# Kernel optimization log

Hardware: AMD Instinct MI355X
Metric: run time of the kernel (lower is better)

The kernel has to match this reference:

```python
import jax, jax.numpy as jnp
import numpy as np

DIM = 320; D_STATE = 32; D_CONV = 4; HEADDIM = 80; D_INNER = 640; NHEADS = 8
CONV_DIM = D_INNER + 2 * D_STATE          # 704
D_IN_PROJ = 2 * D_INNER + 2 * D_STATE + NHEADS  # 1352
ATTN_HEADS = 4; MLP_DIM = 1024; DEPTH = 2; INNER = DIM // 2  # cross-attn downsample_rate=2
PATCH = (128.0, 256.0, 256.0); IMG = (16, 32, 32); NPTS = 6; BATCH = 2
EPS = 1e-5
TWO_PI = 2.0 * np.pi


def layernorm(x, w, b):
    m = x.mean(-1, keepdims=True)
    v = ((x - m) ** 2).mean(-1, keepdims=True)
    return (x - m) * jax.lax.rsqrt(v + EPS) * w + b


def pe_encode(coords, gauss):
    # coords in [0,1], last dim 3 -> random fourier features (sin|cos) of width DIM
    c = TWO_PI * ((2.0 * coords - 1.0) @ gauss)
    return jnp.concatenate([jnp.sin(c), jnp.cos(c)], -1)


def mha(qi, ki, vi, wq, bq, wk, bk, wv, bv, wo, bo):
    q = qi @ wq.T + bq
    k = ki @ wk.T + bk
    v = vi @ wv.T + bv
    B, Nq, Ci = q.shape
    hd = Ci // ATTN_HEADS
    q = q.reshape(B, Nq, ATTN_HEADS, hd)
    k = k.reshape(B, -1, ATTN_HEADS, hd)
    v = v.reshape(B, -1, ATTN_HEADS, hd)
    att = jax.nn.softmax(jnp.einsum('bqhd,bkhd->bhqk', q, k) / np.sqrt(hd), -1)
    o = jnp.einsum('bhqk,bkhd->bqhd', att, v).reshape(B, Nq, Ci)
    return o @ wo.T + bo


def mamba2(xn, in_w, conv_w, conv_b, dt_bias, A_log, Dp, rms_w, out_w):
    Bt, L, _ = xn.shape
    zxbcdt = xn @ in_w.T                                    # (B,L,1352)
    z, xBC, dt = jnp.split(zxbcdt, [D_INNER, D_INNER + CONV_DIM], axis=-1)
    dt = jax.nn.softplus(dt + dt_bias)                      # (B,L,H)
    # causal depthwise conv over sequence, kernel D_CONV
    pad = jnp.pad(xBC, ((0, 0), (D_CONV - 1, 0), (0, 0)))
    conv = conv_b + sum(pad[:, k:k + L] * conv_w[:, k] for k in range(D_CONV))
    xBC = jax.nn.silu(conv)
    xs, Bm, Cm = jnp.split(xBC, [D_INNER, D_INNER + D_STATE], axis=-1)
    A = -jnp.exp(A_log)                                     # (H,)
    xh = xs.reshape(Bt, L, NHEADS, HEADDIM)

    def step(S, inp):  # S: (B,H,N,P)
        dt_t, x_t, B_t, C_t = inp  # (B,H),(B,H,P),(B,N),(B,N)
        decay = jnp.exp(dt_t * A)
        S = S * decay[..., None, None] + (dt_t[..., None, None] * B_t[:, None, :, None]) * x_t[:, :, None, :]
        y = jnp.einsum('bn,bhnp->bhp', C_t, S)
        return S, y

    S0 = jnp.zeros((Bt, NHEADS, D_STATE, HEADDIM), xn.dtype)
    _, ys = jax.lax.scan(step, S0, (dt.transpose(1, 0, 2), xh.transpose(1, 0, 2, 3), Bm.transpose(1, 0, 2), Cm.transpose(1, 0, 2)))
    y = ys.transpose(1, 0, 2, 3) + Dp[None, None, :, None] * xh  # (B,L,H,P)
    y = y.reshape(Bt, L, D_INNER)
    y = y * jax.nn.silu(z)                                  # gated RMSNorm (norm_before_gate=False)
    y = y * jax.lax.rsqrt((y * y).mean(-1, keepdims=True) + EPS) * rms_w
    return y @ out_w.T


def _forward(x, coords, ln_w, ln_b, in_w, conv_w, conv_b, dt_bias, A_log, Dp, rms_w, out_w,
             pe_gauss, point_tab, sa_w, sa_b, t2i_w, t2i_b, t2i_ow, t2i_ob,
             i2t_w, i2t_b, i2t_ow, i2t_ob, norms_w, norms_b, mlp_w1, mlp_b1, mlp_w2, mlp_b2, labels):
    B, C = x.shape[:2]
    img = x.shape[2:]
    n = int(np.prod(img))
    xf = jnp.transpose(x.reshape(B, C, n), (0, 2, 1))       # (B,n,C)
    keys = mamba2(layernorm(xf, ln_w, ln_b), in_w, conv_w, conv_b, dt_bias, A_log, Dp, rms_w, out_w)
    # point embeddings: fourier PE of normalized click coords + label embedding
    point_emb = pe_encode(coords / jnp.asarray(PATCH, x.dtype), pe_gauss) + point_tab[labels]
    # dense image positional encoding over the feature grid
    axes = [(jnp.arange(s, dtype=x.dtype) + 0.5) / s for s in img]
    grid = jnp.stack(jnp.meshgrid(*axes, indexing='ij'), -1)  # (d,h,w,3)
    kpe = jnp.broadcast_to(pe_encode(grid, pe_gauss).reshape(1, n, C), (B, n, C))
    queries = point_emb
    qpe = point_emb
    for i in range(DEPTH):
        saw, sab = sa_w[i], sa_b[i]
        if i == 0:  # skip_first_layer_pe
            queries = mha(queries, queries, queries, saw[0], sab[0], saw[1], sab[1], saw[2], sab[2], saw[3], sab[3])
        else:
            q = queries + qpe
            queries = queries + mha(q, q, queries, saw[0], sab[0], saw[1], sab[1], saw[2], sab[2], saw[3], sab[3])
        queries = layernorm(queries, norms_w[i, 0], norms_b[i, 0])
        q = queries + qpe
        k = keys + kpe
        queries = queries + mha(q, k, keys, t2i_w[i, 0], t2i_b[i, 0], t2i_w[i, 1], t2i_b[i, 1], t2i_w[i, 2], t2i_b[i, 2], t2i_ow[i], t2i_ob[i])
        queries = layernorm(queries, norms_w[i, 1], norms_b[i, 1])
        queries = queries + jax.nn.relu(queries @ mlp_w1[i].T + mlp_b1[i]) @ mlp_w2[i].T + mlp_b2[i]
        queries = layernorm(queries, norms_w[i, 2], norms_b[i, 2])
        q = queries + qpe
        k = keys + kpe
        keys = keys + mha(k, q, queries, i2t_w[i, 0], i2t_b[i, 0], i2t_w[i, 1], i2t_b[i, 1], i2t_w[i, 2], i2t_b[i, 2], i2t_ow[i], i2t_ob[i])
        keys = layernorm(keys, norms_w[i, 3], norms_b[i, 3])
    return jnp.transpose(keys, (0, 2, 1)).reshape(B, C, *img)


def setup_inputs():
    key = jax.random.key(0)
    ks = iter(jax.random.split(key, 64))
    f32 = jnp.float32

    def nrm(shape, s=0.02):
        return s * jax.random.normal(next(ks), shape, dtype=f32)

    inp = {}
    inp['x'] = jax.random.normal(next(ks), (BATCH, DIM) + IMG, dtype=f32)
    inp['coords'] = jax.random.uniform(next(ks), (BATCH, NPTS, 3), dtype=f32) * jnp.asarray(PATCH, f32)
    inp['labels'] = jax.random.randint(next(ks), (BATCH, NPTS), 0, 2)
    inp['ln_w'] = jnp.ones((DIM,), f32)
    inp['ln_b'] = jnp.zeros((DIM,), f32)
    inp['in_w'] = nrm((D_IN_PROJ, DIM))
    inp['conv_w'] = nrm((CONV_DIM, D_CONV), 0.2)
    inp['conv_b'] = jnp.zeros((CONV_DIM,), f32)
    inp['dt_bias'] = nrm((NHEADS,), 0.1)
    inp['A_log'] = jnp.log(jnp.arange(1, NHEADS + 1, dtype=f32))
    inp['Dp'] = jnp.ones((NHEADS,), f32)
    inp['rms_w'] = jnp.ones((D_INNER,), f32)
    inp['out_w'] = nrm((DIM, D_INNER))
    inp['pe_gauss'] = jax.random.normal(next(ks), (3, DIM // 2), dtype=f32)
    inp['point_tab'] = nrm((2, DIM), 1.0)
    inp['sa_w'] = nrm((DEPTH, 4, DIM, DIM))
    inp['sa_b'] = jnp.zeros((DEPTH, 4, DIM), f32)
    inp['t2i_w'] = nrm((DEPTH, 3, INNER, DIM))
    inp['t2i_b'] = jnp.zeros((DEPTH, 3, INNER), f32)
    inp['t2i_ow'] = nrm((DEPTH, DIM, INNER))
    inp['t2i_ob'] = jnp.zeros((DEPTH, DIM), f32)
    inp['i2t_w'] = nrm((DEPTH, 3, INNER, DIM))
    inp['i2t_b'] = jnp.zeros((DEPTH, 3, INNER), f32)
    inp['i2t_ow'] = nrm((DEPTH, DIM, INNER))
    inp['i2t_ob'] = jnp.zeros((DEPTH, DIM), f32)
    inp['norms_w'] = jnp.ones((DEPTH, 4, DIM), f32)
    inp['norms_b'] = jnp.zeros((DEPTH, 4, DIM), f32)
    inp['mlp_w1'] = nrm((DEPTH, MLP_DIM, DIM))
    inp['mlp_b1'] = jnp.zeros((DEPTH, MLP_DIM), f32)
    inp['mlp_w2'] = nrm((DEPTH, DIM, MLP_DIM))
    inp['mlp_b2'] = jnp.zeros((DEPTH, DIM), f32)
    return inp


def reference(x, coords, labels, ln_w, ln_b, in_w, conv_w, conv_b, dt_bias, A_log, Dp, rms_w, out_w,
              pe_gauss, point_tab, sa_w, sa_b, t2i_w, t2i_b, t2i_ow, t2i_ob,
              i2t_w, i2t_b, i2t_ow, i2t_ob, norms_w, norms_b, mlp_w1, mlp_b1, mlp_w2, mlp_b2):
    return _forward(x, coords, ln_w, ln_b, in_w, conv_w, conv_b, dt_bias, A_log, Dp, rms_w, out_w,
                    pe_gauss, point_tab, sa_w, sa_b, t2i_w, t2i_b, t2i_ow, t2i_ob,
                    i2t_w, i2t_b, i2t_ow, i2t_ob, norms_w, norms_b, mlp_w1, mlp_b1, mlp_w2, mlp_b2, labels)
```

## Files before the change

### kernel.cpp

```cpp
#include <hip/hip_runtime.h>
#include <math.h>

#define LSEQ 16384
#define CDIM 320
#define DIN 640
#define NHH 8
#define CONVD 704
#define XBCW 712
#define QCH 64
#define NCHUNK 256

typedef __bf16 bf16_t;
typedef __bf16 bf16x8 __attribute__((ext_vector_type(8)));
typedef __bf16 bf16x4 __attribute__((ext_vector_type(4)));
typedef float f32x4 __attribute__((ext_vector_type(4)));

__device__ __forceinline__ float wave_sum(float v) {
#pragma unroll
  for (int o = 32; o > 0; o >>= 1) v += __shfl_down(v, o, 64);
  return v;
}
__device__ __forceinline__ float wave_max(float v) {
#pragma unroll
  for (int o = 32; o > 0; o >>= 1) v = fmaxf(v, __shfl_down(v, o, 64));
  return v;
}
__device__ __forceinline__ float block_sum256(float v, float* red) {
  int tid = threadIdx.x;
  v = wave_sum(v);
  __syncthreads();
  if ((tid & 63) == 0) red[tid >> 6] = v;
  __syncthreads();
  return red[0] + red[1] + red[2] + red[3];
}

__global__ void ws_probe(float* out, float v) { out[0] = v; }

__global__ void cvt_bf(const float* __restrict__ src, bf16_t* __restrict__ dst, int n) {
  int i = (blockIdx.x * 256 + threadIdx.x) * 4;
  if (i >= n) return;
  float4 v = *(const float4*)(src + i);
  bf16x4 o;
  o[0] = (bf16_t)v.x; o[1] = (bf16_t)v.y; o[2] = (bf16_t)v.z; o[3] = (bf16_t)v.w;
  *(bf16x4*)(dst + i) = o;
}

__global__ __launch_bounds__(256) void tln(const float* __restrict__ x,
                                           const float* __restrict__ w,
                                           const float* __restrict__ b,
                                           bf16_t* __restrict__ out) {
  __shared__ float sT[32][321];
  int t0 = blockIdx.x * 32;
  int tid = threadIdx.x;
  for (int i = tid; i < 2560; i += 256) {
    int c = i >> 3, j4 = i & 7;
    float4 v = *(const float4*)(x + (size_t)c * LSEQ + t0 + j4 * 4);
    sT[j4 * 4 + 0][c] = v.x;
    sT[j4 * 4 + 1][c] = v.y;
    sT[j4 * 4 + 2][c] = v.z;
    sT[j4 * 4 + 3][c] = v.w;
  }
  __syncthreads();
  int wave = tid >> 6, lane = tid & 63;
  for (int tt = wave; tt < 32; tt += 4) {
    float xv[5];
    float s = 0.f;
#pragma unroll
    for (int k = 0; k < 5; ++k) { xv[k] = sT[tt][lane + 64 * k]; s += xv[k]; }
    s = wave_sum(s); s = __shfl(s, 0, 64);
    float mean = s * (1.f / 320.f);
    float v = 0.f;
#pragma unroll
    for (int k = 0; k < 5; ++k) { float d = xv[k] - mean; v += d * d; }
    v = wave_sum(v); v = __shfl(v, 0, 64);
    float rstd = rsqrtf(v * (1.f / 320.f) + 1e-5f);
    bf16_t* op = out + (size_t)(t0 + tt) * CDIM;
#pragma unroll
    for (int k = 0; k < 5; ++k) {
      int i = lane + 64 * k;
      op[i] = (bf16_t)((xv[k] - mean) * rstd * w[i] + b[i]);
    }
  }
}

__global__ __launch_bounds__(256) void lnt(const float* __restrict__ in,
                                           const float* __restrict__ w,
                                           const float* __restrict__ b,
                                           float* __restrict__ out) {
  __shared__ float sT[CDIM][33];
  int t0 = blockIdx.x * 32;
  int tid = threadIdx.x;
  int wave = tid >> 6, lane = tid & 63;
  for (int tt = wave; tt < 32; tt += 4) {
    const float* xp = in + (size_t)(t0 + tt) * CDIM;
    float x[5];
    float s = 0.f;
#pragma unroll
    for (int k = 0; k < 5; ++k) { x[k] = xp[lane + 64 * k]; s += x[k]; }
    s = wave_sum(s); s = __shfl(s, 0, 64);
    float mean = s * (1.f / 320.f);
    float v = 0.f;
#pragma unroll
    for (int k = 0; k < 5; ++k) { float d = x[k] - mean; v += d * d; }
    v = wave_sum(v); v = __shfl(v, 0, 64);
    float rstd = rsqrtf(v * (1.f / 320.f) + 1e-5f);
#pragma unroll
    for (int k = 0; k < 5; ++k) {
      int i = lane + 64 * k;
      sT[i][tt] = (x[k] - mean) * rstd * w[i] + b[i];
    }
  }
  __syncthreads();
  for (int i = tid; i < 320 * 32; i += 256) {
    int cc = i >> 5, t = i & 31;
    out[(size_t)cc * LSEQ + t0 + t] = sT[cc][t];
  }
}

__global__ __launch_bounds__(256) void ln_rows256(float* __restrict__ io,
                                                  const float* __restrict__ w,
                                                  const float* __restrict__ b,
                                                  int nrows) {
  int row = blockIdx.x * 4 + (threadIdx.x >> 6);
  if (row >= nrows) return;
  float* xp = io + (size_t)row * CDIM;
  int lane = threadIdx.x & 63;
  float x[5];
  float s = 0.f;
#pragma unroll
  for (int k = 0; k < 5; ++k) { x[k] = xp[lane + 64 * k]; s += x[k]; }
  s = wave_sum(s); s = __shfl(s, 0, 64);
  float mean = s * (1.f / 320.f);
  float v = 0.f;
#pragma unroll
  for (int k = 0; k < 5; ++k) { float t = x[k] - mean; v += t * t; }
  v = wave_sum(v); v = __shfl(v, 0, 64);
  float rstd = rsqrtf(v * (1.f / 320.f) + 1e-5f);
#pragma unroll
  for (int k = 0; k < 5; ++k) {
    int i = lane + 64 * k;
    xp[i] = (x[k] - mean) * rstd * w[i] + b[i];
  }
}

__global__ __launch_bounds__(256) void gemm64(
    const void* __restrict__ A, const void* __restrict__ W,
    const float* __restrict__ bias, const float* __restrict__ pe,
    void* __restrict__ C, void* __restrict__ C2,
    const void* __restrict__ W2, const float* __restrict__ bias2, int wsplit,
    int M, int N, int K, int lda, int ldc, int nsplit, int ldc2,
    int addC, int abf, int wbf, int cbf, long long sA, long long sC) {
  int z = blockIdx.z;
  int gx = gridDim.x;
  int nwg = gx * gridDim.y;
  int lin = blockIdx.y * gx + blockIdx.x;
  int xcd = lin & 7, idx = lin >> 3;
  int q = nwg >> 3, r = nwg & 7;
  int base = (xcd < r) ? xcd * (q + 1) : r * (q + 1) + (xcd - r) * q;
  int lin2 = base + idx;
  int mblk = lin2 / gx, nblk = lin2 % gx;
  int m0 = mblk << 6, n0 = nblk << 6;

  __shared__ __align__(16) bf16_t As[2][2048];
  __shared__ __align__(16) bf16_t Ws[2][2048];
  int tid = threadIdx.x;
  int wave = tid >> 6, lane = tid & 63;
  int fm = lane & 15, quad = lane >> 4;
  int rA = tid >> 2, qA = tid & 3;
  const float* ag = nullptr;
  const bf16_t* agb = nullptr;
  const float* peg = nullptr;
  if (abf) {
    agb = (const bf16_t*)A + (size_t)z * sA + (size_t)(m0 + rA) * lda + qA * 8;
  } else {
    ag = (const float*)A + (size_t)z * sA + (size_t)(m0 + rA) * lda + qA * 8;
    if (pe) peg = pe + (size_t)(m0 + rA) * lda + qA * 8;
  }
  int wRow = n0 + rA;
  bool wok = wRow < N;
  const float* wg = nullptr;
  const bf16_t* wgb = nullptr;
  {
    const void* Wsel = (wRow < wsplit) ? W : W2;
    int wr = (wRow < wsplit) ? wRow : wRow - wsplit;
    if (wbf) wgb = (const bf16_t*)Wsel + (size_t)wr * K + qA * 8;
    else     wg  = (const float*)Wsel + (size_t)wr * K + qA * 8;
  }
  int off = (rA >> 4) * 512 + (qA * 16 + (rA & 15)) * 8;

  f32x4 acc[4];
#pragma unroll
  for (int j = 0; j < 4; ++j) acc[j] = (f32x4){0.f, 0.f, 0.f, 0.f};

  bf16x8 ra, rw;
  float4 pa0, pa1, pw0, pw1;
  auto loadG = [&](int k0) {
    if (abf) {
      ra = *(const bf16x8*)(agb + k0);
    } else {
      pa0 = *(const float4*)(ag + k0);
      pa1 = *(const float4*)(ag + k0 + 4);
      if (peg) {
        float4 q0 = *(const float4*)(peg + k0);
        float4 q1 = *(const float4*)(peg + k0 + 4);
        pa0.x += q0.x; pa0.y += q0.y; pa0.z += q0.z; pa0.w += q0.w;
        pa1.x += q1.x; pa1.y += q1.y; pa1.z += q1.z; pa1.w += q1.w;
      }
    }
    if (wbf) {
      if (wok) rw = *(const bf16x8*)(wgb + k0);
      else {
#pragma unroll
        for (int j = 0; j < 8; ++j) rw[j] = (bf16_t)0.f;
      }
    } else {
      pw0 = make_float4(0.f, 0.f, 0.f, 0.f);
      pw1 = pw0;
      if (wok) {
        pw0 = *(const float4*)(wg + k0);
        pw1 = *(const float4*)(wg + k0 + 4);
      }
    }
  };
  auto packLDS = [&](int buf) {
    if (!abf) {
      ra[0] = (bf16_t)pa0.x; ra[1] = (bf16_t)pa0.y; ra[2] = (bf16_t)pa0.z; ra[3] = (bf16_t)pa0.w;
      ra[4] = (bf16_t)pa1.x; ra[5] = (bf16_t)pa1.y; ra[6] = (bf16_t)pa1.z; ra[7] = (bf16_t)pa1.w;
    }
    *(bf16x8*)&As[buf][off] = ra;
    if (!wbf) {
      rw[0] = (bf16_t)pw0.x; rw[1] = (bf16_t)pw0.y; rw[2] = (bf16_t)pw0.z; rw[3] = (bf16_t)pw0.w;
      rw[4] = (bf16_t)pw1.x; rw[5] = (bf16_t)pw1.y; rw[6] = (bf16_t)pw1.z; rw[7] = (bf16_t)pw1.w;
    }
    *(bf16x8*)&Ws[buf][off] = rw;
  };

  int nk = K >> 5;
  loadG(0);
  packLDS(0);
  __syncthreads();
  for (int i = 0; i < nk; ++i) {
    int buf = i & 1;
    bool more = (i + 1 < nk);
    if (more) loadG((i + 1) << 5);
    bf16x8 af = *(bf16x8*)&As[buf][wave * 512 + lane * 8];
    bf16x8 b0 = *(bf16x8*)&Ws[buf][lane * 8];
    bf16x8 b1 = *(bf16x8*)&Ws[buf][512 + lane * 8];
    bf16x8 b2 = *(bf16x8*)&Ws[buf][1024 + lane * 8];
    bf16x8 b3 = *(bf16x8*)&Ws[buf][1536 + lane * 8];
    acc[0] = __builtin_amdgcn_mfma_f32_16x16x32_bf16(af, b0, acc[0], 0, 0, 0);
    acc[1] = __builtin_amdgcn_mfma_f32_16x16x32_bf16(af, b1, acc[1], 0, 0, 0);
    acc[2] = __builtin_amdgcn_mfma_f32_16x16x32_bf16(af, b2, acc[2], 0, 0, 0);
    acc[3] = __builtin_amdgcn_mfma_f32_16x16x32_bf16(af, b3, acc[3], 0, 0, 0);
    if (more) {
      packLDS(buf ^ 1);
      __syncthreads();
    }
  }
#pragma unroll
  for (int ns = 0; ns < 4; ++ns) {
    int n = n0 + ns * 16 + fm;
    if (n >= N) continue;
    float bv = 0.f;
    if (n < wsplit) { if (bias) bv = bias[n]; }
    else            { if (bias2) bv = bias2[n - wsplit]; }
    void* Cb;
    int ldcb, nc;
    if (n < nsplit) { Cb = C; ldcb = ldc; nc = n; }
    else            { Cb = C2; ldcb = ldc2; nc = n - nsplit; }
#pragma unroll
    for (int rr = 0; rr < 4; ++rr) {
      int m = m0 + wave * 16 + quad * 4 + rr;
      float v = acc[ns][rr] + bv;
      size_t off2 = (size_t)z * sC + (size_t)m * ldcb + nc;
      if (cbf) {
        ((bf16_t*)Cb)[off2] = (bf16_t)v;
      } else {
        float* Cf = (float*)Cb;
        if (addC) v += Cf[off2];
        Cf[off2] = v;
      }
    }
  }
}

__global__ __launch_bounds__(256) void smallmm(
    const float* __restrict__ A, const float* __restrict__ A2,
    const float* __restrict__ W, const float* __restrict__ bias,
    float* __restrict__ C, int N, int K, int addC, int relu, int a2lim) {
  int wave = threadIdx.x >> 6, lane = threadIdx.x & 63;
  int n = blockIdx.x * 4 + wave;
  if (n >= N) return;
  const float* w = W + (size_t)n * K;
  bool useA2 = (A2 != nullptr) && (n < a2lim);
  float part[12];
#pragma unroll
  for (int m = 0; m < 12; ++m) part[m] = 0.f;
  for (int k0 = 0; k0 < K; k0 += 64) {
    int k = k0 + lane;
    if (k < K) {
      float wv = w[k];
      const float* ap = A + k;
      if (useA2) {
        const float* ap2 = A2 + k;
#pragma unroll
        for (int m = 0; m < 12; ++m)
          part[m] = fmaf(ap[(size_t)m * K] + ap2[(size_t)m * K], wv, part[m]);
      } else {
#pragma unroll
        for (int m = 0; m < 12; ++m)
          part[m] = fmaf(ap[(size_t)m * K], wv, part[m]);
      }
    }
  }
  float bv = bias ? bias[n] : 0.f;
#pragma unroll
  for (int m = 0; m < 12; ++m) {
    float dot = wave_sum(part[m]);
    if (lane == 0) {
      float v = dot + bv;
      if (relu) v = fmaxf(v, 0.f);
      size_t off = (size_t)m * N + n;
      if (addC) v += C[off];
      C[off] = v;
    }
  }
}

__global__ void dt_kernel(const bf16_t* __restrict__ XBC, const float* __restrict__ dt_bias,
                          float* __restrict__ dtbuf) {
  int idx = blockIdx.x * 256 + threadIdx.x;
  if (idx >= LSEQ * NHH) return;
  int h = idx & 7;
  int t = idx >> 3;
  float v = (float)XBC[(size_t)t * XBCW + 704 + h] + dt_bias[h];
  float sp = (v > 20.f) ? v : log1pf(expf(v));
  dtbuf[(size_t)h * LSEQ + t] = sp;
}

__global__ __launch_bounds__(256) void conv2(const bf16_t* __restrict__ XBC,
                                             const float* __restrict__ conv_w,
                                             const float* __restrict__ conv_b,
                                             bf16_t* __restrict__ Cv) {
  int lane = threadIdx.x & 63, wv = threadIdx.x >> 6;
  int d = blockIdx.x * 64 + lane;
  int t0 = (blockIdx.y * 4 + wv) * 32;
  float w0 = conv_w[d * 4 + 0], w1 = conv_w[d * 4 + 1];
  float w2 = conv_w[d * 4 + 2], w3 = conv_w[d * 4 + 3];
  float bv = conv_b[d];
  const bf16_t* src = XBC + d;
  float xm3, xm2, xm1;
  if (t0 == 0) {
    xm3 = 0.f; xm2 = 0.f; xm1 = 0.f;
  } else {
    xm3 = (float)src[(size_t)(t0 - 3) * XBCW];
    xm2 = (float)src[(size_t)(t0 - 2) * XBCW];
    xm1 = (float)src[(size_t)(t0 - 1) * XBCW];
  }
#pragma unroll 8
  for (int t = t0; t < t0 + 32; ++t) {
    float xt = (float)src[(size_t)t * XBCW];
    float a = bv + xm3 * w0 + xm2 * w1 + xm1 * w2 + xt * w3;
    Cv[(size_t)t * CONVD + d] = (bf16_t)(a / (1.f + expf(-a)));
    xm3 = xm2; xm2 = xm1; xm1 = xt;
  }
}

__global__ __launch_bounds__(256) void scan_a(const bf16_t* __restrict__ Cv,
                                              const float* __restrict__ dtbuf,
                                              const float* __restrict__ A_log,
                                              float* __restrict__ Schunk,
                                              float* __restrict__ cabuf) {
  int c = blockIdx.x, h = blockIdx.y;
  int t0 = c * QCH;
  __shared__ float sdt[64], sca[64], sw[64];
  __shared__ __align__(16) float sB[64][36];
  __shared__ __align__(16) float sXt[80][68];
  int tid = threadIdx.x;
  float Aval = -expf(A_log[h]);
  if (tid < 64) sdt[tid] = dtbuf[(size_t)h * LSEQ + t0 + tid];
  __syncthreads();
  if (tid == 0) {
    float run = 0.f;
    for (int j = 0; j < 64; ++j) { run += sdt[j] * Aval; sca[j] = run; }
  }
  __syncthreads();
  float caend = sca[63];
  if (tid < 64) {
    sw[tid] = expf(caend - sca[tid]) * sdt[tid];
    cabuf[(size_t)h * LSEQ + t0 + tid] = sca[tid];
  }
  for (int i = tid; i < 2048; i += 256) {
    int j = i >> 5, n = i & 31;
    sB[j][n] = (float)Cv[(size_t)(t0 + j) * CONVD + 640 + n];
  }
  for (int i = tid; i < 5120; i += 256) {
    int j = i / 80, p = i % 80;
    sXt[p][j] = (float)Cv[(size_t)(t0 + j) * CONVD + h * 80 + p];
  }
  __syncthreads();
  int n = tid >> 3, pb = tid & 7;
  float acc[10];
#pragma unroll
  for (int u = 0; u < 10; ++u) acc[u] = 0.f;
  for (int jb = 0; jb < 16; ++jb) {
    float wB[4];
#pragma unroll
    for (int jj = 0; jj < 4; ++jj) {
      int j = jb * 4 + jj;
      wB[jj] = sw[j] * sB[j][n];
    }
#pragma unroll
    for (int u = 0; u < 10; ++u) {
      int p = pb * 10 + u;
      float4 x4 = *(const float4*)&sXt[p][jb * 4];
      acc[u] += wB[0] * x4.x + wB[1] * x4.y + wB[2] * x4.z + wB[3] * x4.w;
    }
  }
  float* outp = Schunk + (size_t)(h * NCHUNK + c) * 2560;
#pragma unroll
  for (int u = 0; u < 10; ++u) outp[n * 80 + pb * 10 + u] = acc[u];
}

__global__ __launch_bounds__(256) void scan_b(const float* __restrict__ Schunk,
                                              const float* __restrict__ cabuf,
                                              float* __restrict__ Sprev) {
  int pc = blockIdx.x, h = blockIdx.y;
  __shared__ float sdec[256];
  int tid = threadIdx.x;
  sdec[tid] = expf(cabuf[(size_t)h * LSEQ + tid * 64 + 63]);
  __syncthreads();
  int e = pc * 256 + tid;
  const float* base = Schunk + (size_t)h * NCHUNK * 2560 + e;
  float* pbase = Sprev + (size_t)h * NCHUNK * 2560 + e;
  float s = 0.f;
  float v = base[0];
  for (int c = 0; c < NCHUNK; ++c) {
    float vn = (c < NCHUNK - 1) ? base[(size_t)(c + 1) * 2560] : 0.f;
    pbase[(size_t)c * 2560] = s;
    s = s * sdec[c] + v;
    v = vn;
  }
}

__global__ __launch_bounds__(256) void scan_c(const bf16_t* __restrict__ Cv,
                                              const float* __restrict__ dtbuf,
                                              const float* __restrict__ cabuf,
                                              const float* __restrict__ Sprev,
                                              const float* __restrict__ Dp,
                                              bf16_t* __restrict__ Y) {
  int c = blockIdx.x, h = blockIdx.y;
  int t0 = c * QCH;
  __shared__ float sdt[64], sca[64], sexp[64];
  __shared__ __align__(16) bf16_t sC[64 * 40];
  __shared__ __align__(16) bf16_t sB[64 * 40];
  __shared__ __align__(16) bf16_t sXt[80 * 72];
  __shared__ __align__(16) bf16_t sSt[80 * 40];
  __shared__ __align__(16) bf16_t sP[64 * 72];
  int tid = threadIdx.x;
  int wave = tid >> 6, lane = tid & 63;
  int fm = lane & 15, quad = lane >> 4;
  if (tid < 64) {
    sdt[tid] = dtbuf[(size_t)h * LSEQ + t0 + tid];
    float cav = cabuf[(size_t)h * LSEQ + t0 + tid];
    sca[tid] = cav;
    sexp[tid] = expf(cav);
  }
  for (int i = tid; i < 2048; i += 256) {
    int j = i >> 5, n = i & 31;
    size_t base = (size_t)(t0 + j) * CONVD;
    sB[j * 40 + n] = Cv[base + 640 + n];
    sC[j * 40 + n] = Cv[base + 672 + n];
  }
  for (int i = tid; i < 5120; i += 256) {
    int j = i / 80, p = i % 80;
    sXt[p * 72 + j] = Cv[(size_t)(t0 + j) * CONVD + h * 80 + p];
  }
  {
    const float* sp = Sprev + (size_t)(h * NCHUNK + c) * 2560;
    for (int i = tid; i < 2560; i += 256) {
      int n = i / 80, p = i % 80;
      sSt[p * 40 + n] = (bf16_t)sp[i];
    }
  }
  __syncthreads();
  int m0 = wave * 16;
  int jbase = m0 + quad * 4;
  bf16x8 afC = *(bf16x8*)&sC[(m0 + fm) * 40 + quad * 8];
  f32x4 accS[4];
#pragma unroll
  for (int nt = 0; nt < 4; ++nt) {
    bf16x8 bf = *(bf16x8*)&sB[(nt * 16 + fm) * 40 + quad * 8];
    f32x4 zero = (f32x4){0.f, 0.f, 0.f, 0.f};
    accS[nt] = __builtin_amdgcn_mfma_f32_16x16x32_bf16(afC, bf, zero, 0, 0, 0);
  }
  float scaj[4];
#pragma unroll
  for (int r = 0; r < 4; ++r) scaj[r] = sca[jbase + r];
#pragma unroll
  for (int nt = 0; nt < 4; ++nt) {
    int s = nt * 16 + fm;
    float dts = sdt[s], scas = sca[s];
#pragma unroll
    for (int r = 0; r < 4; ++r) {
      int j = jbase + r;
      float v = 0.f;
      if (s <= j) v = accS[nt][r] * dts * expf(scaj[r] - scas);
      sP[j * 72 + s] = (bf16_t)v;
    }
  }
  f32x4 acc[5];
#pragma unroll
  for (int pt = 0; pt < 5; ++pt) {
    bf16x8 bf = *(bf16x8*)&sSt[(pt * 16 + fm) * 40 + quad * 8];
    f32x4 zero = (f32x4){0.f, 0.f, 0.f, 0.f};
    acc[pt] = __builtin_amdgcn_mfma_f32_16x16x32_bf16(afC, bf, zero, 0, 0, 0);
  }
  float gj[4];
#pragma unroll
  for (int r = 0; r < 4; ++r) gj[r] = sexp[jbase + r];
#pragma unroll
  for (int pt = 0; pt < 5; ++pt)
#pragma unroll
    for (int r = 0; r < 4; ++r) acc[pt][r] *= gj[r];
  bf16x8 afP0 = *(bf16x8*)&sP[(m0 + fm) * 72 + 0 + quad * 8];
  bf16x8 afP1 = *(bf16x8*)&sP[(m0 + fm) * 72 + 32 + quad * 8];
#pragma unroll
  for (int pt = 0; pt < 5; ++pt) {
    bf16x8 bx0 = *(bf16x8*)&sXt[(pt * 16 + fm) * 72 + 0 + quad * 8];
    bf16x8 bx1 = *(bf16x8*)&sXt[(pt * 16 + fm) * 72 + 32 + quad * 8];
    acc[pt] = __builtin_amdgcn_mfma_f32_16x16x32_bf16(afP0, bx0, acc[pt], 0, 0, 0);
    acc[pt] = __builtin_amdgcn_mfma_f32_16x16x32_bf16(afP1, bx1, acc[pt], 0, 0, 0);
  }
  float dval = Dp[h];
#pragma unroll
  for (int pt = 0; pt < 5; ++pt) {
    int p = pt * 16 + fm;
#pragma unroll
    for (int r = 0; r < 4; ++r) {
      int j = jbase + r;
      float xv = (float)sXt[p * 72 + j];
      Y[(size_t)(t0 + j) * DIN + h * 80 + p] = (bf16_t)(acc[pt][r] + dval * xv);
    }
  }
}

__global__ __launch_bounds__(256) void gate_rms(bf16_t* __restrict__ YS,
                                                const bf16_t* __restrict__ Z,
                                                const float* __restrict__ rms_w) {
  __shared__ float red[4];
  size_t row = blockIdx.x;
  bf16_t* y = YS + row * DIN;
  const bf16_t* z = Z + row * DIN;
  int tid = threadIdx.x;
  float g0, g1, g2 = 0.f;
  {
    float zi = (float)z[tid];
    g0 = (float)y[tid] * (zi / (1.f + expf(-zi)));
    zi = (float)z[tid + 256];
    g1 = (float)y[tid + 256] * (zi / (1.f + expf(-zi)));
    if (tid + 512 < DIN) {
      zi = (float)z[tid + 512];
      g2 = (float)y[tid + 512] * (zi / (1.f + expf(-zi)));
    }
  }
  float ss = g0 * g0 + g1 * g1 + g2 * g2;
  float tot = block_sum256(ss, red);
  float r = rsqrtf(tot / (float)DIN + 1e-5f);
  y[tid] = (bf16_t)(g0 * r * rms_w[tid]);
  y[tid + 256] = (bf16_t)(g1 * r * rms_w[tid + 256]);
  if (tid + 512 < DIN) y[tid + 512] = (bf16_t)(g2 * r * rms_w[tid + 512]);
}

__global__ void kpe_kernel(const float* __restrict__ gauss, float* __restrict__ KPE) {
  int idx = blockIdx.x * 256 + threadIdx.x;
  if (idx >= LSEQ * 160) return;
  int f = idx % 160, t = idx / 160;
  int d = t >> 10, hh = (t >> 5) & 31, w = t & 31;
  float vx = 2.f * ((d + 0.5f) / 16.f) - 1.f;
  float vy = 2.f * ((hh + 0.5f) / 32.f) - 1.f;
  float vz = 2.f * ((w + 0.5f) / 32.f) - 1.f;
  float cc = 6.28318530717958647692f * (vx * gauss[f] + vy * gauss[160 + f] + vz * gauss[320 + f]);
  KPE[(size_t)t * CDIM + f] = sinf(cc);
  KPE[(size_t)t * CDIM + 160 + f] = cosf(cc);
}

__global__ void point_kernel(const float* __restrict__ coords, const int* __restrict__ labels,
                             const float* __restrict__ gauss, const float* __restrict__ ptab,
                             float* __restrict__ qpe, float* __restrict__ queries) {
  int idx = blockIdx.x * 64 + threadIdx.x;
  if (idx >= 12 * 160) return;
  int f = idx % 160, pt = idx / 160;
  const float* co = coords + pt * 3;
  float vx = 2.f * (co[0] / 128.f) - 1.f;
  float vy = 2.f * (co[1] / 256.f) - 1.f;
  float vz = 2.f * (co[2] / 256.f) - 1.f;
  float cc = 6.28318530717958647692f * (vx * gauss[f] + vy * gauss[160 + f] + vz * gauss[320 + f]);
  int lab = labels[pt];
  float sv = sinf(cc) + ptab[lab * CDIM + f];
  float cv = cosf(cc) + ptab[lab * CDIM + 160 + f];
  qpe[pt * CDIM + f] = sv;       qpe[pt * CDIM + 160 + f] = cv;
  queries[pt * CDIM + f] = sv;   queries[pt * CDIM + 160 + f] = cv;
}

__global__ void attn_self(const float* __restrict__ P3, float* __restrict__ O) {
  int h = blockIdx.x, b = blockIdx.y;
  __shared__ float sq[6][80], sk[6][80], sv[6][80], sw[6][6];
  int tid = threadIdx.x;
  for (int i = tid; i < 480; i += 128) {
    int tok = i / 80, p = i % 80;
    const float* base = P3 + (size_t)(b * 6 + tok) * 960 + h * 80 + p;
    sq[tok][p] = base[0]; sk[tok][p] = base[320]; sv[tok][p] = base[640];
  }
  __syncthreads();
  if (tid < 36) {
    int qi = tid / 6, ki = tid % 6;
    float d = 0.f;
    for (int p = 0; p < 80; ++p) d += sq[qi][p] * sk[ki][p];
    sw[qi][ki] = d * 0.11180339887498948f;
  }
  __syncthreads();
  if (tid < 6) {
    float mx = sw[tid][0];
    for (int k = 1; k < 6; ++k) mx = fmaxf(mx, sw[tid][k]);
    float s = 0.f;
    for (int k = 0; k < 6; ++k) { float e = expf(sw[tid][k] - mx); sw[tid][k] = e; s += e; }
    float inv = 1.f / s;
    for (int k = 0; k < 6; ++k) sw[tid][k] *= inv;
  }
  __syncthreads();
  for (int i = tid; i < 480; i += 128) {
    int qi = i / 80, p = i % 80;
    float o = 0.f;
    for (int k = 0; k < 6; ++k) o += sw[qi][k] * sv[k][p];
    O[(size_t)(b * 6 + qi) * CDIM + h * 80 + p] = o;
  }
}

__global__ __launch_bounds__(256) void attn_t2i_part2(const float* __restrict__ Qp,
                                                      const bf16_t* __restrict__ Kp,
                                                      const bf16_t* __restrict__ Vp,
                                                      float* __restrict__ Part) {
  int b = blockIdx.z, h = blockIdx.y, c = blockIdx.x;
  Qp += (size_t)b * 960;
  Kp += (size_t)b * LSEQ * 160;
  Vp += (size_t)b * LSEQ * 160;
  Part += (size_t)b * 24 * 64 * 42;
  __shared__ float sq[240];
  __shared__ float redm[4][6], reds[4][6];
  __shared__ __align__(16) bf16_t sPb[16 * 264];
  __shared__ __align__(16) bf16_t sVtb[48 * 264];
  int tid = threadIdx.x;
  int wave = tid >> 6, lane = tid & 63;
  if (tid < 240) sq[tid] = Qp[(size_t)(tid / 40) * 160 + h * 40 + (tid % 40)];
  __syncthreads();
  int t = c * 256 + tid;
  const bf16_t* kp = Kp + (size_t)t * 160 + h * 40;
  float kr[40];
#pragma unroll
  for (int v = 0; v < 5; ++v) {
    bf16x8 k8 = *(const bf16x8*)(kp + v * 8);
#pragma unroll
    for (int j = 0; j < 8; ++j) kr[v * 8 + j] = (float)k8[j];
  }
  const bf16_t* vp = Vp + (size_t)t * 160 + h * 40;
#pragma unroll
  for (int v = 0; v < 5; ++v) {
    bf16x8 v8 = *(const bf16x8*)(vp + v * 8);
#pragma unroll
    for (int j = 0; j < 8; ++j) sVtb[(v * 8 + j) * 264 + tid] = v8[j];
  }
  float s[6];
#pragma unroll
  for (int qi = 0; qi < 6; ++qi) {
    float d = 0.f;
#pragma unroll
    for (int p = 0; p < 40; ++p) d += sq[qi * 40 + p] * kr[p];
    s[qi] = d * 0.15811388300841897f;
  }
#pragma unroll
  for (int qi = 0; qi < 6; ++qi) {
    float wm = wave_max(s[qi]);
    if (lane == 0) redm[wave][qi] = wm;
  }
  __syncthreads();
  float gmax[6], ls[6];
#pragma unroll
  for (int qi = 0; qi < 6; ++qi)
    gmax[qi] = fmaxf(fmaxf(redm[0][qi], redm[1][qi]), fmaxf(redm[2][qi], redm[3][qi]));
#pragma unroll
  for (int qi = 0; qi < 6; ++qi) {
    float e = expf(s[qi] - gmax[qi]);
    sPb[qi * 264 + tid] = (bf16_t)e;
    float wsum = wave_sum(e);
    if (lane == 0) reds[wave][qi] = wsum;
  }
  __syncthreads();
#pragma unroll
  for (int qi = 0; qi < 6; ++qi)
    ls[qi] = reds[0][qi] + reds[1][qi] + reds[2][qi] + reds[3][qi];
  if (tid == 0) {
#pragma unroll
    for (int qi = 0; qi < 6; ++qi) {
      float* pml = Part + (size_t)((h * 6 + qi) * 64 + c) * 42;
      pml[40] = gmax[qi];
      pml[41] = ls[qi];
    }
  }
  if (wave == 0) {
    int fm = lane & 15, quad = lane >> 4;
    f32x4 acc[3];
#pragma unroll
    for (int nt = 0; nt < 3; ++nt) acc[nt] = (f32x4){0.f, 0.f, 0.f, 0.f};
#pragma unroll
    for (int ks = 0; ks < 8; ++ks) {
      bf16x8 a = *(bf16x8*)&sPb[fm * 264 + ks * 32 + quad * 8];
#pragma unroll
      for (int nt = 0; nt < 3; ++nt) {
        bf16x8 bb = *(bf16x8*)&sVtb[(nt * 16 + fm) * 264 + ks * 32 + quad * 8];
        acc[nt] = __builtin_amdgcn_mfma_f32_16x16x32_bf16(a, bb, acc[nt], 0, 0, 0);
      }
    }
#pragma unroll
    for (int nt = 0; nt < 3; ++nt)
#pragma unroll
      for (int r = 0; r < 4; ++r) {
        int qi = quad * 4 + r;
        int p = nt * 16 + fm;
        if (qi < 6 && p < 40)
          Part[(size_t)((h * 6 + qi) * 64 + c) * 42 + p] = acc[nt][r];
      }
  }
}

__global__ void attn_t2i_comb(const float* __restrict__ Part, float* __restrict__ O) {
  int b = blockIdx.y;
  int blk = blockIdx.x;
  int qi = blk % 6;
  int h = blk / 6;
  int j = threadIdx.x;
  const float* base = Part + (size_t)b * 24 * 64 * 42 + (size_t)blk * 64 * 42;
  float m = base[j * 42 + 40], l = base[j * 42 + 41];
  float gmax = wave_max(m);
  gmax = __shfl(gmax, 0, 64);
  float sc = expf(m - gmax);
  float tot = wave_sum(l * sc);
  tot = __shfl(tot, 0, 64);
  float inv = 1.f / tot;
  __shared__ float ssc[64];
  ssc[j] = sc;
  __syncthreads();
  if (j < 40) {
    float a0 = 0.f, a1 = 0.f, a2 = 0.f, a3 = 0.f;
    for (int jj = 0; jj < 64; jj += 4) {
      a0 = fmaf(base[(jj + 0) * 42 + j], ssc[jj + 0], a0);
      a1 = fmaf(base[(jj + 1) * 42 + j], ssc[jj + 1], a1);
      a2 = fmaf(base[(jj + 2) * 42 + j], ssc[jj + 2], a2);
      a3 = fmaf(base[(jj + 3) * 42 + j], ssc[jj + 3], a3);
    }
    O[(size_t)b * 960 + (size_t)qi * 160 + h * 40 + j] = (a0 + a1 + a2 + a3) * inv;
  }
}

__global__ __launch_bounds__(256) void attn_i2t(const bf16_t* __restrict__ Qp,
                                                const float* __restrict__ KV,
                                                bf16_t* __restrict__ O) {
  int h = blockIdx.y, b = blockIdx.z;
  int t = blockIdx.x * 256 + threadIdx.x;
  Qp += (size_t)b * LSEQ * 160;
  O += (size_t)b * LSEQ * 160;
  __shared__ float sk[6][40], sv[6][40];
  if (threadIdx.x < 240) {
    int tok = threadIdx.x / 40, p = threadIdx.x % 40;
    const float* base = KV + (size_t)(b * 6 + tok) * 320 + h * 40 + p;
    sk[tok][p] = base[0];
    sv[tok][p] = base[160];
  }
  __syncthreads();
  const bf16_t* q = Qp + (size_t)t * 160 + h * 40;
  float qr[40];
#pragma unroll
  for (int v = 0; v < 5; ++v) {
    bf16x8 q8 = *(const bf16x8*)(q + v * 8);
#pragma unroll
    for (int j = 0; j < 8; ++j) qr[v * 8 + j] = (float)q8[j];
  }
  float s[6];
#pragma unroll
  for (int k = 0; k < 6; ++k) {
    float d = 0.f;
    for (int p = 0; p < 40; ++p) d += qr[p] * sk[k][p];
    s[k] = d * 0.15811388300841897f;
  }
  float mx = s[0];
#pragma unroll
  for (int k = 1; k < 6; ++k) mx = fmaxf(mx, s[k]);
  float sum = 0.f;
#pragma unroll
  for (int k = 0; k < 6; ++k) { s[k] = expf(s[k] - mx); sum += s[k]; }
  float inv = 1.f / sum;
  bf16_t* o = O + (size_t)t * 160 + h * 40;
#pragma unroll
  for (int v = 0; v < 10; ++v) {
    float o0 = 0.f, o1 = 0.f, o2 = 0.f, o3 = 0.f;
#pragma unroll
    for (int k = 0; k < 6; ++k) {
      float w = s[k];
      o0 += w * sv[k][v * 4 + 0];
      o1 += w * sv[k][v * 4 + 1];
      o2 += w * sv[k][v * 4 + 2];
      o3 += w * sv[k][v * 4 + 3];
    }
    bf16x4 ov;
    ov[0] = (bf16_t)(o0 * inv); ov[1] = (bf16_t)(o1 * inv);
    ov[2] = (bf16_t)(o2 * inv); ov[3] = (bf16_t)(o3 * inv);
    *(bf16x4*)(o + v * 4) = ov;
  }
}

extern "C" void kernel_launch(void* const* d_in, const int* in_sizes, int n_in,
                              void* d_out, int out_size, void* d_ws, size_t ws_size,
                              hipStream_t stream) {
  (void)in_sizes; (void)n_in; (void)out_size;
  const float* x       = (const float*)d_in[0];
  const float* coords  = (const float*)d_in[1];
  const int*   labels  = (const int*)  d_in[2];
  const float* ln_w    = (const float*)d_in[3];
  const float* ln_b    = (const float*)d_in[4];
  const float* in_w    = (const float*)d_in[5];
  const float* conv_w  = (const float*)d_in[6];
  const float* conv_b  = (const float*)d_in[7];
  const float* dt_bias = (const float*)d_in[8];
  const float* A_log   = (const float*)d_in[9];
  const float* Dp      = (const float*)d_in[10];
  const float* rms_w   = (const float*)d_in[11];
  const float* out_w   = (const float*)d_in[12];
  const float* gauss   = (const float*)d_in[13];
  const float* ptab    = (const float*)d_in[14];
  const float* sa_w    = (const float*)d_in[15];
  const float* sa_b    = (const float*)d_in[16];
  const float* t2i_w   = (const float*)d_in[17];
  const float* t2i_b   = (const float*)d_in[18];
  const float* t2i_ow  = (const float*)d_in[19];
  const float* t2i_ob  = (const float*)d_in[20];
  const float* i2t_w   = (const float*)d_in[21];
  const float* i2t_b   = (const float*)d_in[22];
  const float* i2t_ow  = (const float*)d_in[23];
  const float* i2t_ob  = (const float*)d_in[24];
  const float* norms_w = (const float*)d_in[25];
  const float* norms_b = (const float*)d_in[26];
  const float* mlp_w1  = (const float*)d_in[27];
  const float* mlp_b1  = (const float*)d_in[28];
  const float* mlp_w2  = (const float*)d_in[29];
  const float* mlp_b2  = (const float*)d_in[30];
  float* out = (float*)d_out;
  float* ws = (float*)d_ws;

  const size_t NEED = (size_t)(10485760 + 5242880 + 11665408 + 11534336 + 10485760 +
                               131072 + 131072 + 65536) * 4;
  if (ws_size < NEED) {
    ws_probe<<<1, 1, 0, stream>>>(out, (float)ws_size);
    return;
  }
  float* R_K = ws;
  float* P   = ws + 10485760;
  bf16_t* XNB_   = (bf16_t*)P;
  float* SCHUNK_ = P;
  bf16_t* ZBB_   = (bf16_t*)(P + 5242880);
  bf16_t* XBCB_  = (bf16_t*)(P + 10485760);
  float* SPREV_  = P + 10485760;
  bf16_t* CVB_   = (bf16_t*)(P + 16318464);
  bf16_t* YSB_   = (bf16_t*)(P + 22085632);
  float* DT_     = P + 27328512;
  float* CA_     = P + 27459584;
  bf16_t* WBI_   = (bf16_t*)(P + 27590656);
  bf16_t* WBO_   = (bf16_t*)(P + 27806976);
  float* KPE_   = P;
  bf16_t* T0B_  = (bf16_t*)(P + 5242880);
  bf16_t* T3B_  = (bf16_t*)(P + 7864320);
  bf16_t* T1B_  = (bf16_t*)(P + 10485760);
  bf16_t* T2B_  = (bf16_t*)(P + 13107200);
  float* PART_  = P + 15728640;
  float* SM_    = P + 15857664;
  float* QPE_  = SM_;
  float* QRY_  = SM_ + 3840;
  float* P3_   = SM_ + 7680;
  float* PO_   = SM_ + 19200;
  float* H_    = SM_ + 23040;
  float* Q160_ = SM_ + 35328;
  float* O160_ = SM_ + 37248;
  float* KV_   = SM_ + 39168;

  const long long sIMG160 = (long long)LSEQ * 160;
  const long long sIMG320 = (long long)LSEQ * CDIM;
  const int NOSPLIT = 1 << 30;

  cvt_bf<<<(432640 / 4 + 255) / 256, 256, 0, stream>>>(in_w, WBI_, 432640);
  cvt_bf<<<(204800 / 4 + 255) / 256, 256, 0, stream>>>(out_w, WBO_, 204800);

  for (int b = 0; b < 2; ++b) {
    const float* xb = x + (size_t)b * CDIM * LSEQ;
    float* Kb = R_K + (size_t)b * LSEQ * CDIM;

    tln<<<LSEQ / 32, 256, 0, stream>>>(xb, ln_w, ln_b, XNB_);

    gemm64<<<dim3(22, 256, 1), 256, 0, stream>>>(
        XNB_, WBI_, nullptr, nullptr, ZBB_, XBCB_, nullptr, nullptr, NOSPLIT,
        LSEQ, 1352, CDIM, CDIM, DIN, DIN, XBCW, 0, 1, 1, 1, 0, 0);

    dt_kernel<<<LSEQ * NHH / 256, 256, 0, stream>>>(XBCB_, dt_bias, DT_);
    conv2<<<dim3(11, 128), 256, 0, stream>>>(XBCB_, conv_w, conv_b, CVB_);

    scan_a<<<dim3(NCHUNK, NHH), 256, 0, stream>>>(CVB_, DT_, A_log, SCHUNK_, CA_);
    scan_b<<<dim3(10, NHH), 256, 0, stream>>>(SCHUNK_, CA_, SPREV_);
    scan_c<<<dim3(NCHUNK, NHH), 256, 0, stream>>>(CVB_, DT_, CA_, SPREV_, Dp, YSB_);

    gate_rms<<<LSEQ, 256, 0, stream>>>(YSB_, ZBB_, rms_w);

    gemm64<<<dim3(5, 256, 1), 256, 0, stream>>>(
        YSB_, WBO_, nullptr, nullptr, Kb, nullptr, nullptr, nullptr, NOSPLIT,
        LSEQ, CDIM, DIN, DIN, CDIM, NOSPLIT, 0, 0, 1, 1, 0, 0, 0);
  }

  kpe_kernel<<<LSEQ * 160 / 256, 256, 0, stream>>>(gauss, KPE_);
  point_kernel<<<30, 64, 0, stream>>>(coords, labels, gauss, ptab, QPE_, QRY_);

  for (int i = 0; i < 2; ++i) {
    const float* saw = sa_w + (size_t)i * 4 * CDIM * CDIM;
    const float* sab = sa_b + (size_t)i * 4 * CDIM;
    smallmm<<<240, 256, 0, stream>>>(QRY_, (i == 0) ? nullptr : QPE_,
                                     saw, sab, P3_, 960, CDIM, 0, 0, 640);
    attn_self<<<dim3(4, 2), 128, 0, stream>>>(P3_, PO_);
    smallmm<<<80, 256, 0, stream>>>(PO_, nullptr, saw + 3 * 102400, sab + 3 * CDIM,
                                    QRY_, CDIM, CDIM, (i == 0) ? 0 : 1, 0, 0);
    ln_rows256<<<3, 256, 0, stream>>>(QRY_, norms_w + (size_t)(i * 4 + 0) * CDIM,
                                      norms_b + (size_t)(i * 4 + 0) * CDIM, 12);

    smallmm<<<40, 256, 0, stream>>>(QRY_, QPE_, t2i_w + (size_t)(i * 3 + 0) * 51200,
                                    t2i_b + (size_t)(i * 3 + 0) * 160, Q160_,
                                    160, CDIM, 0, 0, 160);
    gemm64<<<dim3(5, 256, 2), 256, 0, stream>>>(
        R_K, t2i_w + (size_t)(i * 3 + 1) * 51200, t2i_b + (size_t)(i * 3 + 1) * 160,
        KPE_, T0B_, T3B_, i2t_w + (size_t)(i * 3 + 0) * 51200,
        i2t_b + (size_t)(i * 3 + 0) * 160, 160,
        LSEQ, 320, CDIM, CDIM, 160, 160, 160, 0, 0, 0, 1, sIMG320, sIMG160);
    gemm64<<<dim3(3, 256, 2), 256, 0, stream>>>(
        R_K, t2i_w + (size_t)(i * 3 + 2) * 51200, t2i_b + (size_t)(i * 3 + 2) * 160,
        nullptr, T1B_, nullptr, nullptr, nullptr, NOSPLIT,
        LSEQ, 160, CDIM, CDIM, 160, NOSPLIT, 0, 0, 0, 0, 1, sIMG320, sIMG160);
    attn_t2i_part2<<<dim3(64, 4, 2), 256, 0, stream>>>(Q160_, T0B_, T1B_, PART_);
    attn_t2i_comb<<<dim3(24, 2), 64, 0, stream>>>(PART_, O160_);
    smallmm<<<80, 256, 0, stream>>>(O160_, nullptr, t2i_ow + (size_t)i * 51200,
                                    t2i_ob + (size_t)i * CDIM, QRY_,
                                    CDIM, 160, 1, 0, 0);
    ln_rows256<<<3, 256, 0, stream>>>(QRY_, norms_w + (size_t)(i * 4 + 1) * CDIM,
                                      norms_b + (size_t)(i * 4 + 1) * CDIM, 12);

    smallmm<<<256, 256, 0, stream>>>(QRY_, nullptr, mlp_w1 + (size_t)i * 1024 * CDIM,
                                     mlp_b1 + (size_t)i * 1024, H_, 1024, CDIM, 0, 1, 0);
    smallmm<<<80, 256, 0, stream>>>(H_, nullptr, mlp_w2 + (size_t)i * CDIM * 1024,
                                    mlp_b2 + (size_t)i * CDIM, QRY_, CDIM, 1024, 1, 0, 0);
    ln_rows256<<<3, 256, 0, stream>>>(QRY_, norms_w + (size_t)(i * 4 + 2) * CDIM,
                                      norms_b + (size_t)(i * 4 + 2) * CDIM, 12);

    smallmm<<<80, 256, 0, stream>>>(QRY_, QPE_, i2t_w + (size_t)(i * 3 + 1) * 51200,
                                    i2t_b + (size_t)(i * 3 + 1) * 160, KV_,
                                    320, CDIM, 0, 0, 160);
    attn_i2t<<<dim3(LSEQ / 256, 4, 2), 256, 0, stream>>>(T3B_, KV_, T2B_);
    gemm64<<<dim3(5, 256, 2), 256, 0, stream>>>(
        T2B_, i2t_ow + (size_t)i * CDIM * 160, i2t_ob + (size_t)i * CDIM,
        nullptr, R_K, nullptr, nullptr, nullptr, NOSPLIT,
        LSEQ, CDIM, 160, 160, CDIM, NOSPLIT, 0, 1, 1, 0, 0, sIMG160, sIMG320);
    if (i == 0) {
      ln_rows256<<<2 * LSEQ / 4, 256, 0, stream>>>(
          R_K, norms_w + (size_t)3 * CDIM, norms_b + (size_t)3 * CDIM, 2 * LSEQ);
    }
  }

  for (int b = 0; b < 2; ++b) {
    lnt<<<LSEQ / 32, 256, 0, stream>>>(
        R_K + (size_t)b * LSEQ * CDIM, norms_w + (size_t)7 * CDIM,
        norms_b + (size_t)7 * CDIM, out + (size_t)b * CDIM * LSEQ);
  }
}
```

Before: 966.3 us.

## Replace LDS double-buffered GEMM with direct-load MFMA GEMM using XCD-aware block remap

Adds a gemmd kernel that loads A and W fragments straight from global memory into MFMA operands, skipping LDS staging and the per-iteration barriers. It also remaps block IDs so consecutive tiles land on the same XCD for L2 locality. All three large GEMM call sites switch to it. Without LDS, each wave loads the W tile separately, so the kernel relies on cache hits and adds global traffic and latency exposure.

```diff
diff --git a/kernel.cpp b/kernel.cpp
--- a/kernel.cpp
+++ b/kernel.cpp
@@ -256,6 +256,103 @@
       packLDS(buf ^ 1);
       __syncthreads();
     }
+  }
+#pragma unroll
+  for (int ns = 0; ns < 4; ++ns) {
+    int n = n0 + ns * 16 + fm;
+    if (n >= N) continue;
+    float bv = 0.f;
+    if (n < wsplit) { if (bias) bv = bias[n]; }
+    else            { if (bias2) bv = bias2[n - wsplit]; }
+    void* Cb;
+    int ldcb, nc;
+    if (n < nsplit) { Cb = C; ldcb = ldc; nc = n; }
+    else            { Cb = C2; ldcb = ldc2; nc = n - nsplit; }
+#pragma unroll
+    for (int rr = 0; rr < 4; ++rr) {
+      int m = m0 + wave * 16 + quad * 4 + rr;
+      float v = acc[ns][rr] + bv;
+      size_t off2 = (size_t)z * sC + (size_t)m * ldcb + nc;
+      if (cbf) {
+        ((bf16_t*)Cb)[off2] = (bf16_t)v;
+      } else {
+        float* Cf = (float*)Cb;
+        if (addC) v += Cf[off2];
+        Cf[off2] = v;
+      }
+    }
+  }
+}
+
+__global__ __launch_bounds__(256) void gemmd(
+    const bf16_t* __restrict__ A, const void* __restrict__ W,
+    const float* __restrict__ bias,
+    void* __restrict__ C, void* __restrict__ C2,
+    const void* __restrict__ W2, const float* __restrict__ bias2, int wsplit,
+    int M, int N, int K, int lda, int ldc, int nsplit, int ldc2,
+    int addC, int wbf, int cbf, long long sA, long long sC) {
+  int z = blockIdx.z;
+  int gx = gridDim.x;
+  int nwg = gx * gridDim.y;
+  int lin = blockIdx.y * gx + blockIdx.x;
+  int xcd = lin & 7, idx = lin >> 3;
+  int q = nwg >> 3, r = nwg & 7;
+  int base = (xcd < r) ? xcd * (q + 1) : r * (q + 1) + (xcd - r) * q;
+  int lin2 = base + idx;
+  int mblk = lin2 / gx, nblk = lin2 % gx;
+  int m0 = mblk << 6, n0 = nblk << 6;
+  int tid = threadIdx.x;
+  int wave = tid >> 6, lane = tid & 63;
+  int fm = lane & 15, quad = lane >> 4;
+  const bf16_t* ap = A + (size_t)z * sA + (size_t)(m0 + wave * 16 + fm) * lda + quad * 8;
+  const bf16_t* wpb[4];
+  const float* wpf[4];
+  bool ok[4];
+#pragma unroll
+  for (int nt = 0; nt < 4; ++nt) {
+    int wRow = n0 + nt * 16 + fm;
+    ok[nt] = wRow < N;
+    int wr2 = ok[nt] ? wRow : 0;
+    const void* Wsel = (wr2 < wsplit) ? W : W2;
+    int wr = (wr2 < wsplit) ? wr2 : wr2 - wsplit;
+    if (wbf) wpb[nt] = (const bf16_t*)Wsel + (size_t)wr * K + quad * 8;
+    else     wpf[nt] = (const float*)Wsel + (size_t)wr * K + quad * 8;
+  }
+  f32x4 acc[4];
+#pragma unroll
+  for (int j = 0; j < 4; ++j) acc[j] = (f32x4){0.f, 0.f, 0.f, 0.f};
+
+#pragma unroll 2
+  for (int k0 = 0; k0 < K; k0 += 32) {
+    bf16x8 a = *(const bf16x8*)(ap + k0);
+    bf16x8 b0, b1, b2, b3;
+    if (wbf) {
+      b0 = *(const bf16x8*)(wpb[0] + k0);
+      b1 = *(const bf16x8*)(wpb[1] + k0);
+      b2 = *(const bf16x8*)(wpb[2] + k0);
+      b3 = *(const bf16x8*)(wpb[3] + k0);
+    } else {
+      float4 w00 = *(const float4*)(wpf[0] + k0);
+      float4 w01 = *(const float4*)(wpf[0] + k0 + 4);
+      float4 w10 = *(const float4*)(wpf[1] + k0);
+      float4 w11 = *(const float4*)(wpf[1] + k0 + 4);
+      float4 w20 = *(const float4*)(wpf[2] + k0);
+      float4 w21 = *(const float4*)(wpf[2] + k0 + 4);
+      float4 w30 = *(const float4*)(wpf[3] + k0);
+      float4 w31 = *(const float4*)(wpf[3] + k0 + 4);
+      b0[0] = (bf16_t)w00.x; b0[1] = (bf16_t)w00.y; b0[2] = (bf16_t)w00.z; b0[3] = (bf16_t)w00.w;
+      b0[4] = (bf16_t)w01.x; b0[5] = (bf16_t)w01.y; b0[6] = (bf16_t)w01.z; b0[7] = (bf16_t)w01.w;
+      b1[0] = (bf16_t)w10.x; b1[1] = (bf16_t)w10.y; b1[2] = (bf16_t)w10.z; b1[3] = (bf16_t)w10.w;
+      b1[4] = (bf16_t)w11.x; b1[5] = (bf16_t)w11.y; b1[6] = (bf16_t)w11.z; b1[7] = (bf16_t)w11.w;
+      b2[0] = (bf16_t)w20.x; b2[1] = (bf16_t)w20.y; b2[2] = (bf16_t)w20.z; b2[3] = (bf16_t)w20.w;
+      b2[4] = (bf16_t)w21.x; b2[5] = (bf16_t)w21.y; b2[6] = (bf16_t)w21.z; b2[7] = (bf16_t)w21.w;
+      b3[0] = (bf16_t)w30.x; b3[1] = (bf16_t)w30.y; b3[2] = (bf16_t)w30.z; b3[3] = (bf16_t)w30.w;
+      b3[4] = (bf16_t)w31.x; b3[5] = (bf16_t)w31.y; b3[6] = (bf16_t)w31.z; b3[7] = (bf16_t)w31.w;
+    }
+    acc[0] = __builtin_amdgcn_mfma_f32_16x16x32_bf16(a, b0, acc[0], 0, 0, 0);
+    acc[1] = __builtin_amdgcn_mfma_f32_16x16x32_bf16(a, b1, acc[1], 0, 0, 0);
+    acc[2] = __builtin_amdgcn_mfma_f32_16x16x32_bf16(a, b2, acc[2], 0, 0, 0);
+    acc[3] = __builtin_amdgcn_mfma_f32_16x16x32_bf16(a, b3, acc[3], 0, 0, 0);
   }
 #pragma unroll
   for (int ns = 0; ns < 4; ++ns) {
@@ -904,9 +1001,9 @@
 
     tln<<<LSEQ / 32, 256, 0, stream>>>(xb, ln_w, ln_b, XNB_);
 
-    gemm64<<<dim3(22, 256, 1), 256, 0, stream>>>(
-        XNB_, WBI_, nullptr, nullptr, ZBB_, XBCB_, nullptr, nullptr, NOSPLIT,
-        LSEQ, 1352, CDIM, CDIM, DIN, DIN, XBCW, 0, 1, 1, 1, 0, 0);
+    gemmd<<<dim3(22, 256, 1), 256, 0, stream>>>(
+        XNB_, WBI_, nullptr, ZBB_, XBCB_, nullptr, nullptr, NOSPLIT,
+        LSEQ, 1352, CDIM, CDIM, DIN, DIN, XBCW, 0, 1, 1, 0, 0);
 
     dt_kernel<<<LSEQ * NHH / 256, 256, 0, stream>>>(XBCB_, dt_bias, DT_);
     conv2<<<dim3(11, 128), 256, 0, stream>>>(XBCB_, conv_w, conv_b, CVB_);
@@ -917,9 +1014,9 @@
 
     gate_rms<<<LSEQ, 256, 0, stream>>>(YSB_, ZBB_, rms_w);
 
-    gemm64<<<dim3(5, 256, 1), 256, 0, stream>>>(
-        YSB_, WBO_, nullptr, nullptr, Kb, nullptr, nullptr, nullptr, NOSPLIT,
-        LSEQ, CDIM, DIN, DIN, CDIM, NOSPLIT, 0, 0, 1, 1, 0, 0, 0);
+    gemmd<<<dim3(5, 256, 1), 256, 0, stream>>>(
+        YSB_, WBO_, nullptr, Kb, nullptr, nullptr, nullptr, NOSPLIT,
+        LSEQ, CDIM, DIN, DIN, CDIM, NOSPLIT, 0, 0, 1, 0, 0, 0);
   }
 
   kpe_kernel<<<LSEQ * 160 / 256, 256, 0, stream>>>(gauss, KPE_);
@@ -967,10 +1064,10 @@
                                     i2t_b + (size_t)(i * 3 + 1) * 160, KV_,
                                     320, CDIM, 0, 0, 160);
     attn_i2t<<<dim3(LSEQ / 256, 4, 2), 256, 0, stream>>>(T3B_, KV_, T2B_);
-    gemm64<<<dim3(5, 256, 2), 256, 0, stream>>>(
+    gemmd<<<dim3(5, 256, 2), 256, 0, stream>>>(
         T2B_, i2t_ow + (size_t)i * CDIM * 160, i2t_ob + (size_t)i * CDIM,
-        nullptr, R_K, nullptr, nullptr, nullptr, NOSPLIT,
-        LSEQ, CDIM, 160, 160, CDIM, NOSPLIT, 0, 1, 1, 0, 0, sIMG160, sIMG320);
+        R_K, nullptr, nullptr, nullptr, NOSPLIT,
+        LSEQ, CDIM, 160, 160, CDIM, NOSPLIT, 0, 1, 0, 0, sIMG160, sIMG320);
     if (i == 0) {
       ln_rows256<<<2 * LSEQ / 4, 256, 0, stream>>>(
           R_K, norms_w + (size_t)3 * CDIM, norms_b + (size_t)3 * CDIM, 2 * LSEQ);
```

Result: slower. 1.315 ms (+36.0%).
